# Performance work log

Measured on AMD Instinct MI355X. Metric: run time of the kernel, lower is better.

Reference implementation:

```python
import jax, jax.numpy as jnp
import numpy as np

N = 50000      # B*N nodes
K = 32         # top-k in-degree
E = N * K      # edges
IN_DIM = 128
EMB_DIM = 128
OUT_DIM = 128
HEADS = 4
D_HEAD = OUT_DIM // HEADS


def setup_inputs() -> dict:
    key = jax.random.key(0)
    ks = jax.random.split(key, 8)
    x = jax.random.normal(ks[0], (N, IN_DIM), dtype=jnp.float32)
    emb = jax.random.normal(ks[1], (N, EMB_DIM), dtype=jnp.float32)
    # top-k graph: each node i has exactly K in-neighbors (dst covers all nodes)
    dst = jnp.repeat(jnp.arange(N, dtype=jnp.int32), K)
    src = jax.random.randint(ks[2], (E,), 0, N, dtype=jnp.int32)
    edge_index = jnp.stack([src, dst], axis=0)
    # learned params (stored as (in, out); math-equivalent to torch Linear)
    W_q = jax.random.normal(ks[3], (EMB_DIM, OUT_DIM), dtype=jnp.float32) / np.sqrt(EMB_DIM)
    W_k = jax.random.normal(ks[4], (EMB_DIM, OUT_DIM), dtype=jnp.float32) / np.sqrt(EMB_DIM)
    W_v = jax.random.normal(ks[5], (IN_DIM + EMB_DIM, OUT_DIM), dtype=jnp.float32) / np.sqrt(IN_DIM + EMB_DIM)
    attn_vec = jax.random.normal(ks[6], (HEADS, 2 * D_HEAD), dtype=jnp.float32) / np.sqrt(2 * D_HEAD)
    ln_gamma = jnp.ones((OUT_DIM,), dtype=jnp.float32)
    ln_beta = jnp.zeros((OUT_DIM,), dtype=jnp.float32)
    return {"x": x, "emb": emb, "edge_index": edge_index, "W_q": W_q, "W_k": W_k,
            "W_v": W_v, "attn_vec": attn_vec, "ln_gamma": ln_gamma, "ln_beta": ln_beta}


def reference(x, emb, edge_index, W_q, W_k, W_v, attn_vec, ln_gamma, ln_beta):
    src, dst = edge_index[0], edge_index[1]
    BN = x.shape[0]
    H, D = HEADS, D_HEAD
    Q = (emb @ W_q).reshape(BN, H, D)
    K_ = (emb @ W_k).reshape(BN, H, D)
    # a^T [q_dst || k_src] = (a_q . q)_dst + (a_k . k)_src  (standard GAT split)
    a_q, a_k = attn_vec[:, :D], attn_vec[:, D:]
    sq = jnp.einsum('nhd,hd->nh', Q, a_q)   # (BN, H)
    sk = jnp.einsum('nhd,hd->nh', K_, a_k)  # (BN, H)
    e = sq[dst] + sk[src]                   # (E, H)
    e = jnp.where(e > 0, e, 0.2 * e)        # LeakyReLU(0.2)
    # segment softmax over incoming edges of each dst node
    e_max = jax.ops.segment_max(e, dst, num_segments=BN)
    e_exp = jnp.exp(e - e_max[dst])
    e_sum = jax.ops.segment_sum(e_exp, dst, num_segments=BN)
    alpha = e_exp / (e_sum[dst] + 1e-8)     # (E, H); dropout is identity at eval
    V = (jnp.concatenate([x, emb], axis=-1) @ W_v).reshape(BN, H, D)
    weighted = alpha[..., None] * V[src]    # (E, H, D)
    z = jax.ops.segment_sum(weighted, dst, num_segments=BN).reshape(BN, H * D)
    z = jax.nn.elu(z)
    mu = jnp.mean(z, axis=-1, keepdims=True)
    var = jnp.var(z, axis=-1, keepdims=True)
    return (z - mu) / jnp.sqrt(var + 1e-5) * ln_gamma + ln_beta
```

## Files before the change

kernel.cpp:

```cpp
#include <hip/hip_runtime.h>

#define NN 50000
#define KE 32

using f32x4  = __attribute__((ext_vector_type(4))) float;
using bf16x8 = __attribute__((ext_vector_type(8))) short;

__device__ __forceinline__ ushort f2bf(float f) {
    union { float f; unsigned u; } c; c.f = f;
    unsigned u = c.u;
    u += 0x7fffu + ((u >> 16) & 1u);
    return (ushort)(u >> 16);
}

__global__ __launch_bounds__(256) void prep_kernel(const float* __restrict__ Wq,
        const float* __restrict__ Wk, const float* __restrict__ av,
        const float* __restrict__ Wv, ushort* __restrict__ Ub,
        ushort* __restrict__ Bt) {
    const int g = blockIdx.x * 256 + threadIdx.x;
    if (blockIdx.x < 2) {
        const int h = g >> 7, i = g & 127;
        float su = 0.f, sv = 0.f;
#pragma unroll
        for (int d = 0; d < 32; ++d) {
            su += Wq[i * 128 + h * 32 + d] * av[h * 64 + d];
            sv += Wk[i * 128 + h * 32 + d] * av[h * 64 + 32 + d];
        }
        Ub[h * 128 + i] = f2bf(su);
        Ub[(4 + h) * 128 + i] = f2bf(sv);
        Ub[1024 + g * 2] = 0;
        Ub[1024 + g * 2 + 1] = 0;
    } else {
        const int idx = g - 512;
        const int k = idx >> 7, n = idx & 127;
        Bt[n * 256 + k] = f2bf(Wv[idx]);
    }
}

__global__ __launch_bounds__(256) void vproj_mfma(const float* __restrict__ x,
        const float* __restrict__ emb, const ushort* __restrict__ Bt,
        const ushort* __restrict__ Ub, float* __restrict__ sq,
        float* __restrict__ sk, ushort* __restrict__ Vb) {
    __shared__ short As[64 * 264];
    const int t = threadIdx.x;
    const int rbase = blockIdx.x * 64;

#pragma unroll
    for (int it = 0; it < 16; ++it) {
        const int li = it * 256 + t;
        const int row = li >> 6;
        const int c4 = li & 63;
        int rg = rbase + row; if (rg >= NN) rg = NN - 1;
        const float* sp = (c4 < 32) ? (x + (long)rg * 128 + c4 * 4)
                                    : (emb + (long)rg * 128 + (c4 - 32) * 4);
        float4 a = *(const float4*)sp;
        ushort4 b = make_ushort4(f2bf(a.x), f2bf(a.y), f2bf(a.z), f2bf(a.w));
        *(ushort4*)&As[row * 264 + c4 * 4] = b;
    }
    __syncthreads();

    const int wv = t >> 6;
    const int lane = t & 63;
    const int lo = lane & 15;
    const int quad = lane >> 4;
    const int c0 = wv * 32;

    f32x4 acc[4][2] = {};
    for (int ks = 0; ks < 8; ++ks) {
        const int kb = ks * 32 + quad * 8;
        bf16x8 bf0 = *(const bf16x8*)(Bt + (c0 + lo) * 256 + kb);
        bf16x8 bf1 = *(const bf16x8*)(Bt + (c0 + 16 + lo) * 256 + kb);
#pragma unroll
        for (int rt = 0; rt < 4; ++rt) {
            bf16x8 af = *(const bf16x8*)&As[(rt * 16 + lo) * 264 + kb];
            acc[rt][0] = __builtin_amdgcn_mfma_f32_16x16x32_bf16(af, bf0, acc[rt][0], 0, 0, 0);
            acc[rt][1] = __builtin_amdgcn_mfma_f32_16x16x32_bf16(af, bf1, acc[rt][1], 0, 0, 0);
        }
    }

    f32x4 sacc = {};
#pragma unroll
    for (int ks = 0; ks < 4; ++ks) {
        const int kk = ks * 32 + quad * 8;
        bf16x8 saf = *(const bf16x8*)&As[(wv * 16 + lo) * 264 + 128 + kk];
        bf16x8 sbf = *(const bf16x8*)(Ub + lo * 128 + kk);
        sacc = __builtin_amdgcn_mfma_f32_16x16x32_bf16(saf, sbf, sacc, 0, 0, 0);
    }
    if (lo < 8) {
#pragma unroll
        for (int r = 0; r < 4; ++r) {
            const int row = rbase + wv * 16 + quad * 4 + r;
            if (row < NN) {
                if (lo < 4) sq[(long)row * 4 + lo] = sacc[r];
                else        sk[(long)row * 4 + lo - 4] = sacc[r];
            }
        }
    }

    __syncthreads();
#pragma unroll
    for (int rt = 0; rt < 4; ++rt)
#pragma unroll
        for (int ct = 0; ct < 2; ++ct)
#pragma unroll
            for (int r = 0; r < 4; ++r)
                As[(rt * 16 + quad * 4 + r) * 132 + c0 + ct * 16 + lo] =
                    (short)f2bf(acc[rt][ct][r]);
    __syncthreads();
#pragma unroll
    for (int i = 0; i < 4; ++i) {
        const int idx = i * 256 + t;
        const int row = idx >> 4;
        const int seg = idx & 15;
        const int grow = rbase + row;
        if (grow < NN)
            *(bf16x8*)(Vb + (long)grow * 128 + seg * 8) =
                *(const bf16x8*)&As[row * 132 + seg * 8];
    }
}

__global__ __launch_bounds__(256) void aggregate_kernel(const int* __restrict__ src,
        const float* __restrict__ sq, const float* __restrict__ sk,
        const ushort* __restrict__ Vb, const float* __restrict__ gamma,
        const float* __restrict__ beta, float* __restrict__ out) {
    __shared__ int s_src[4][32];
    __shared__ float4 s_alpha[4][32];
    const int w = threadIdx.x >> 6;
    const int lane = threadIdx.x & 63;
    const int n = blockIdx.x * 4 + w;

    if (lane < 32) {
        const int s = src[(long)n * KE + lane];
        float4 sk4 = *(const float4*)(sk + (long)s * 4);
        float4 sq4 = *(const float4*)(sq + (long)n * 4);
        float e[4] = { sq4.x + sk4.x, sq4.y + sk4.y, sq4.z + sk4.z, sq4.w + sk4.w };
#pragma unroll
        for (int h = 0; h < 4; ++h) e[h] = e[h] > 0.f ? e[h] : 0.2f * e[h];
        float m[4] = { e[0], e[1], e[2], e[3] };
#pragma unroll
        for (int off = 16; off > 0; off >>= 1) {
#pragma unroll
            for (int h = 0; h < 4; ++h) m[h] = fmaxf(m[h], __shfl_xor(m[h], off));
        }
        float ex[4], sum[4];
#pragma unroll
        for (int h = 0; h < 4; ++h) { ex[h] = __expf(e[h] - m[h]); sum[h] = ex[h]; }
#pragma unroll
        for (int off = 16; off > 0; off >>= 1) {
#pragma unroll
            for (int h = 0; h < 4; ++h) sum[h] += __shfl_xor(sum[h], off);
        }
        float4 al;
        al.x = ex[0] / (sum[0] + 1e-8f);
        al.y = ex[1] / (sum[1] + 1e-8f);
        al.z = ex[2] / (sum[2] + 1e-8f);
        al.w = ex[3] / (sum[3] + 1e-8f);
        s_src[w][lane] = s;
        s_alpha[w][lane] = al;
    }
    __syncthreads();

    const int g  = lane >> 4;
    const int li = lane & 15;
    const int h  = li >> 2;
    float z[8] = {};
#pragma unroll
    for (int it = 0; it < 8; ++it) {
        const int e = it * 4 + g;
        const int s = s_src[w][e];
        const float a = ((const float*)&s_alpha[w][e])[h];
        uint4 p = *(const uint4*)(Vb + (long)s * 128 + li * 8);
        const unsigned pc[4] = { p.x, p.y, p.z, p.w };
#pragma unroll
        for (int j = 0; j < 4; ++j) {
            union { unsigned u; float f; } ve, vo;
            ve.u = pc[j] << 16;
            vo.u = pc[j] & 0xffff0000u;
            z[2 * j]     += a * ve.f;
            z[2 * j + 1] += a * vo.f;
        }
    }
#pragma unroll
    for (int j = 0; j < 8; ++j) {
        z[j] += __shfl_xor(z[j], 16);
        z[j] += __shfl_xor(z[j], 32);
    }
    float s1 = 0.f, s2 = 0.f;
#pragma unroll
    for (int j = 0; j < 8; ++j) {
        z[j] = z[j] > 0.f ? z[j] : __expf(z[j]) - 1.f;
        s1 += z[j];
        s2 += z[j] * z[j];
    }
#pragma unroll
    for (int off = 8; off > 0; off >>= 1) {
        s1 += __shfl_xor(s1, off);
        s2 += __shfl_xor(s2, off);
    }
    const float mu = s1 * (1.f / 128.f);
    const float var = s2 * (1.f / 128.f) - mu * mu;
    const float rstd = rsqrtf(var + 1e-5f);
    if (g < 2) {
        const int c0 = li * 8 + g * 4;
        float4 ga = *(const float4*)(gamma + c0);
        float4 be = *(const float4*)(beta + c0);
        float4 o;
        o.x = (z[g * 4 + 0] - mu) * rstd * ga.x + be.x;
        o.y = (z[g * 4 + 1] - mu) * rstd * ga.y + be.y;
        o.z = (z[g * 4 + 2] - mu) * rstd * ga.z + be.z;
        o.w = (z[g * 4 + 3] - mu) * rstd * ga.w + be.w;
        *(float4*)(out + (long)n * 128 + c0) = o;
    }
}

extern "C" void kernel_launch(void* const* d_in, const int* in_sizes, int n_in,
                              void* d_out, int out_size, void* d_ws, size_t ws_size,
                              hipStream_t stream) {
    const float* x     = (const float*)d_in[0];
    const float* emb   = (const float*)d_in[1];
    const int*   edge  = (const int*)d_in[2];
    const float* Wq    = (const float*)d_in[3];
    const float* Wk    = (const float*)d_in[4];
    const float* Wv    = (const float*)d_in[5];
    const float* av    = (const float*)d_in[6];
    const float* gamma = (const float*)d_in[7];
    const float* beta  = (const float*)d_in[8];
    float* out = (float*)d_out;

    char* ws = (char*)d_ws;
    ushort* Ub = (ushort*)(ws + 0);
    ushort* Bt = (ushort*)(ws + 4096);
    float*  sq = (float*)(ws + 69632);
    float*  sk = (float*)(ws + 869632);
    ushort* Vb = (ushort*)(ws + 1669632);

    prep_kernel<<<130, 256, 0, stream>>>(Wq, Wk, av, Wv, Ub, Bt);
    vproj_mfma<<<(NN + 63) / 64, 256, 0, stream>>>(x, emb, Bt, Ub, sq, sk, Vb);
    aggregate_kernel<<<NN / 4, 256, 0, stream>>>(edge, sq, sk, Vb, gamma, beta, out);
}
```

Baseline: 178.2 us.

## Split aggregation into alpha, per-head gather, and layernorm kernels with head-planar V

The fused aggregate kernel becomes three passes. An alpha kernel writes fp16 attention weights per edge. A gather kernel works on one head plane at a time, so the gathered V rows are 64-byte head slices and each head's working set is smaller and more cache-friendly. A final kernel applies ELU and layer norm in place. V is stored head-planar, and the Bt fragments are hoisted into registers before the barrier. The cost is extra launches plus the round trips of alpha and z through global memory, and fp16 alpha adds some rounding error.

```diff
diff --git a/kernel.cpp b/kernel.cpp
--- a/kernel.cpp
+++ b/kernel.cpp
@@ -2,6 +2,7 @@
 
 #define NN 50000
 #define KE 32
+#define PAD_N 50048
 
 using f32x4  = __attribute__((ext_vector_type(4))) float;
 using bf16x8 = __attribute__((ext_vector_type(8))) short;
@@ -11,6 +12,12 @@
     unsigned u = c.u;
     u += 0x7fffu + ((u >> 16) & 1u);
     return (ushort)(u >> 16);
+}
+__device__ __forceinline__ ushort f2h(float f) {
+    union { _Float16 h; ushort u; } c; c.h = (_Float16)f; return c.u;
+}
+__device__ __forceinline__ float h2f(ushort u) {
+    union { ushort u; _Float16 h; } c; c.u = u; return (float)c.h;
 }
 
 __global__ __launch_bounds__(256) void prep_kernel(const float* __restrict__ Wq,
@@ -40,10 +47,15 @@
 __global__ __launch_bounds__(256) void vproj_mfma(const float* __restrict__ x,
         const float* __restrict__ emb, const ushort* __restrict__ Bt,
         const ushort* __restrict__ Ub, float* __restrict__ sq,
-        float* __restrict__ sk, ushort* __restrict__ Vb) {
+        float* __restrict__ sk, ushort* __restrict__ Vp) {
     __shared__ short As[64 * 264];
     const int t = threadIdx.x;
     const int rbase = blockIdx.x * 64;
+    const int wv = t >> 6;
+    const int lane = t & 63;
+    const int lo = lane & 15;
+    const int quad = lane >> 4;
+    const int c0 = wv * 32;
 
 #pragma unroll
     for (int it = 0; it < 16; ++it) {
@@ -57,24 +69,24 @@
         ushort4 b = make_ushort4(f2bf(a.x), f2bf(a.y), f2bf(a.z), f2bf(a.w));
         *(ushort4*)&As[row * 264 + c4 * 4] = b;
     }
-    __syncthreads();
-
-    const int wv = t >> 6;
-    const int lane = t & 63;
-    const int lo = lane & 15;
-    const int quad = lane >> 4;
-    const int c0 = wv * 32;
-
-    f32x4 acc[4][2] = {};
+    bf16x8 bt0[8], bt1[8];
+#pragma unroll
     for (int ks = 0; ks < 8; ++ks) {
         const int kb = ks * 32 + quad * 8;
-        bf16x8 bf0 = *(const bf16x8*)(Bt + (c0 + lo) * 256 + kb);
-        bf16x8 bf1 = *(const bf16x8*)(Bt + (c0 + 16 + lo) * 256 + kb);
+        bt0[ks] = *(const bf16x8*)(Bt + (c0 + lo) * 256 + kb);
+        bt1[ks] = *(const bf16x8*)(Bt + (c0 + 16 + lo) * 256 + kb);
+    }
+    __syncthreads();
+
+    f32x4 acc[4][2] = {};
+#pragma unroll
+    for (int ks = 0; ks < 8; ++ks) {
+        const int kb = ks * 32 + quad * 8;
 #pragma unroll
         for (int rt = 0; rt < 4; ++rt) {
             bf16x8 af = *(const bf16x8*)&As[(rt * 16 + lo) * 264 + kb];
-            acc[rt][0] = __builtin_amdgcn_mfma_f32_16x16x32_bf16(af, bf0, acc[rt][0], 0, 0, 0);
-            acc[rt][1] = __builtin_amdgcn_mfma_f32_16x16x32_bf16(af, bf1, acc[rt][1], 0, 0, 0);
+            acc[rt][0] = __builtin_amdgcn_mfma_f32_16x16x32_bf16(af, bt0[ks], acc[rt][0], 0, 0, 0);
+            acc[rt][1] = __builtin_amdgcn_mfma_f32_16x16x32_bf16(af, bt1[ks], acc[rt][1], 0, 0, 0);
         }
     }
 
@@ -113,104 +125,113 @@
         const int row = idx >> 4;
         const int seg = idx & 15;
         const int grow = rbase + row;
+        const int plane = seg >> 2;
+        const int pc = (seg & 3) * 8;
         if (grow < NN)
-            *(bf16x8*)(Vb + (long)grow * 128 + seg * 8) =
+            *(bf16x8*)(Vp + (long)plane * PAD_N * 32 + (long)grow * 32 + pc) =
                 *(const bf16x8*)&As[row * 132 + seg * 8];
     }
 }
 
-__global__ __launch_bounds__(256) void aggregate_kernel(const int* __restrict__ src,
+__global__ __launch_bounds__(256) void alpha_kernel(const int* __restrict__ src,
         const float* __restrict__ sq, const float* __restrict__ sk,
-        const ushort* __restrict__ Vb, const float* __restrict__ gamma,
-        const float* __restrict__ beta, float* __restrict__ out) {
-    __shared__ int s_src[4][32];
-    __shared__ float4 s_alpha[4][32];
+        ushort* __restrict__ alpha) {
+    const int t = threadIdx.x;
+    const int e = t & 31;
+    const int n = blockIdx.x * 8 + (t >> 5);
+    const int s = src[(long)n * KE + e];
+    float4 sk4 = *(const float4*)(sk + (long)s * 4);
+    float4 sq4 = *(const float4*)(sq + (long)n * 4);
+    float ev[4] = { sq4.x + sk4.x, sq4.y + sk4.y, sq4.z + sk4.z, sq4.w + sk4.w };
+#pragma unroll
+    for (int h = 0; h < 4; ++h) ev[h] = ev[h] > 0.f ? ev[h] : 0.2f * ev[h];
+    float m[4] = { ev[0], ev[1], ev[2], ev[3] };
+#pragma unroll
+    for (int off = 16; off > 0; off >>= 1) {
+#pragma unroll
+        for (int h = 0; h < 4; ++h) m[h] = fmaxf(m[h], __shfl_xor(m[h], off));
+    }
+    float ex[4], sum[4];
+#pragma unroll
+    for (int h = 0; h < 4; ++h) { ex[h] = __expf(ev[h] - m[h]); sum[h] = ex[h]; }
+#pragma unroll
+    for (int off = 16; off > 0; off >>= 1) {
+#pragma unroll
+        for (int h = 0; h < 4; ++h) sum[h] += __shfl_xor(sum[h], off);
+    }
+#pragma unroll
+    for (int h = 0; h < 4; ++h)
+        alpha[(long)n * 128 + h * 32 + e] = f2h(ex[h] / (sum[h] + 1e-8f));
+}
+
+__global__ __launch_bounds__(256) void gather_kernel(const int* __restrict__ src,
+        const ushort* __restrict__ alpha, const ushort* __restrict__ Vp,
+        float* __restrict__ z) {
+    __shared__ int   s_src[32 * 33];
+    __shared__ float s_al [32 * 33];
+    const int b = blockIdx.x;
+    const int head = (b & 7) >> 1;
+    const int chunk = (b >> 3) * 2 + (b & 1);
+    const int nbase = chunk * 32;
+    const int t = threadIdx.x;
+
+#pragma unroll
+    for (int i = 0; i < 4; ++i) {
+        const int idx = i * 256 + t;
+        const int n = idx >> 5, e = idx & 31;
+        const int nn = nbase + n;
+        s_src[n * 33 + e] = (nn < NN) ? src[(long)nn * KE + e] : 0;
+        const ushort a = (nn < NN) ? alpha[(long)nn * 128 + head * 32 + e] : 0;
+        s_al[n * 33 + e] = h2f(a);
+    }
+    __syncthreads();
+
+    const int slot = t >> 3;
+    const int l = t & 7;
+    const int node = nbase + slot;
+    const ushort* plane = Vp + (long)head * PAD_N * 32;
+    float z0 = 0.f, z1 = 0.f, z2 = 0.f, z3 = 0.f;
+#pragma unroll 8
+    for (int e = 0; e < 32; ++e) {
+        const int sidx = s_src[slot * 33 + e];
+        const float a = s_al[slot * 33 + e];
+        uint2 p = *(const uint2*)(plane + (long)sidx * 32 + l * 4);
+        union { unsigned u; float f; } e0, o0, e1, o1;
+        e0.u = p.x << 16; o0.u = p.x & 0xffff0000u;
+        e1.u = p.y << 16; o1.u = p.y & 0xffff0000u;
+        z0 += a * e0.f; z1 += a * o0.f; z2 += a * e1.f; z3 += a * o1.f;
+    }
+    if (node < NN)
+        *(float4*)(z + (long)node * 128 + head * 32 + l * 4) =
+            make_float4(z0, z1, z2, z3);
+}
+
+__global__ __launch_bounds__(256) void lnorm_kernel(float* __restrict__ z,
+        const float* __restrict__ gamma, const float* __restrict__ beta) {
     const int w = threadIdx.x >> 6;
     const int lane = threadIdx.x & 63;
     const int n = blockIdx.x * 4 + w;
-
-    if (lane < 32) {
-        const int s = src[(long)n * KE + lane];
-        float4 sk4 = *(const float4*)(sk + (long)s * 4);
-        float4 sq4 = *(const float4*)(sq + (long)n * 4);
-        float e[4] = { sq4.x + sk4.x, sq4.y + sk4.y, sq4.z + sk4.z, sq4.w + sk4.w };
-#pragma unroll
-        for (int h = 0; h < 4; ++h) e[h] = e[h] > 0.f ? e[h] : 0.2f * e[h];
-        float m[4] = { e[0], e[1], e[2], e[3] };
-#pragma unroll
-        for (int off = 16; off > 0; off >>= 1) {
-#pragma unroll
-            for (int h = 0; h < 4; ++h) m[h] = fmaxf(m[h], __shfl_xor(m[h], off));
-        }
-        float ex[4], sum[4];
-#pragma unroll
-        for (int h = 0; h < 4; ++h) { ex[h] = __expf(e[h] - m[h]); sum[h] = ex[h]; }
-#pragma unroll
-        for (int off = 16; off > 0; off >>= 1) {
-#pragma unroll
-            for (int h = 0; h < 4; ++h) sum[h] += __shfl_xor(sum[h], off);
-        }
-        float4 al;
-        al.x = ex[0] / (sum[0] + 1e-8f);
-        al.y = ex[1] / (sum[1] + 1e-8f);
-        al.z = ex[2] / (sum[2] + 1e-8f);
-        al.w = ex[3] / (sum[3] + 1e-8f);
-        s_src[w][lane] = s;
-        s_alpha[w][lane] = al;
-    }
-    __syncthreads();
-
-    const int g  = lane >> 4;
-    const int li = lane & 15;
-    const int h  = li >> 2;
-    float z[8] = {};
-#pragma unroll
-    for (int it = 0; it < 8; ++it) {
-        const int e = it * 4 + g;
-        const int s = s_src[w][e];
-        const float a = ((const float*)&s_alpha[w][e])[h];
-        uint4 p = *(const uint4*)(Vb + (long)s * 128 + li * 8);
-        const unsigned pc[4] = { p.x, p.y, p.z, p.w };
-#pragma unroll
-        for (int j = 0; j < 4; ++j) {
-            union { unsigned u; float f; } ve, vo;
-            ve.u = pc[j] << 16;
-            vo.u = pc[j] & 0xffff0000u;
-            z[2 * j]     += a * ve.f;
-            z[2 * j + 1] += a * vo.f;
-        }
-    }
-#pragma unroll
-    for (int j = 0; j < 8; ++j) {
-        z[j] += __shfl_xor(z[j], 16);
-        z[j] += __shfl_xor(z[j], 32);
-    }
-    float s1 = 0.f, s2 = 0.f;
-#pragma unroll
-    for (int j = 0; j < 8; ++j) {
-        z[j] = z[j] > 0.f ? z[j] : __expf(z[j]) - 1.f;
-        s1 += z[j];
-        s2 += z[j] * z[j];
-    }
-#pragma unroll
-    for (int off = 8; off > 0; off >>= 1) {
+    const int c0 = lane * 2;
+    float2 zv = *(const float2*)(z + (long)n * 128 + c0);
+    float zx = zv.x, zy = zv.y;
+    zx = zx > 0.f ? zx : __expf(zx) - 1.f;
+    zy = zy > 0.f ? zy : __expf(zy) - 1.f;
+    float s1 = zx + zy;
+    float s2 = zx * zx + zy * zy;
+#pragma unroll
+    for (int off = 32; off > 0; off >>= 1) {
         s1 += __shfl_xor(s1, off);
         s2 += __shfl_xor(s2, off);
     }
     const float mu = s1 * (1.f / 128.f);
     const float var = s2 * (1.f / 128.f) - mu * mu;
     const float rstd = rsqrtf(var + 1e-5f);
-    if (g < 2) {
-        const int c0 = li * 8 + g * 4;
-        float4 ga = *(const float4*)(gamma + c0);
-        float4 be = *(const float4*)(beta + c0);
-        float4 o;
-        o.x = (z[g * 4 + 0] - mu) * rstd * ga.x + be.x;
-        o.y = (z[g * 4 + 1] - mu) * rstd * ga.y + be.y;
-        o.z = (z[g * 4 + 2] - mu) * rstd * ga.z + be.z;
-        o.w = (z[g * 4 + 3] - mu) * rstd * ga.w + be.w;
-        *(float4*)(out + (long)n * 128 + c0) = o;
-    }
+    float2 g = *(const float2*)(gamma + c0);
+    float2 b = *(const float2*)(beta + c0);
+    float2 o;
+    o.x = (zx - mu) * rstd * g.x + b.x;
+    o.y = (zy - mu) * rstd * g.y + b.y;
+    *(float2*)(z + (long)n * 128 + c0) = o;
 }
 
 extern "C" void kernel_launch(void* const* d_in, const int* in_sizes, int n_in,
@@ -228,13 +249,16 @@
     float* out = (float*)d_out;
 
     char* ws = (char*)d_ws;
-    ushort* Ub = (ushort*)(ws + 0);
-    ushort* Bt = (ushort*)(ws + 4096);
-    float*  sq = (float*)(ws + 69632);
-    float*  sk = (float*)(ws + 869632);
-    ushort* Vb = (ushort*)(ws + 1669632);
+    ushort* Ub    = (ushort*)(ws + 0);
+    ushort* Bt    = (ushort*)(ws + 4096);
+    float*  sq    = (float*)(ws + 69632);
+    float*  sk    = (float*)(ws + 869632);
+    ushort* alpha = (ushort*)(ws + 1669632);
+    ushort* Vp    = (ushort*)(ws + 14469632);
 
     prep_kernel<<<130, 256, 0, stream>>>(Wq, Wk, av, Wv, Ub, Bt);
-    vproj_mfma<<<(NN + 63) / 64, 256, 0, stream>>>(x, emb, Bt, Ub, sq, sk, Vb);
-    aggregate_kernel<<<NN / 4, 256, 0, stream>>>(edge, sq, sk, Vb, gamma, beta, out);
-}
+    vproj_mfma<<<(NN + 63) / 64, 256, 0, stream>>>(x, emb, Bt, Ub, sq, sk, Vp);
+    alpha_kernel<<<NN / 8, 256, 0, stream>>>(edge, sq, sk, alpha);
+    gather_kernel<<<782 * 8, 256, 0, stream>>>(edge, alpha, Vp, out);
+    lnorm_kernel<<<NN / 4, 256, 0, stream>>>(out, gamma, beta);
+}
```

Measured after the change: 196.1 us. +10.1%, slower.
